# Kernel optimization log

Hardware: AMD Instinct MI355X
Metric: run time of the kernel (lower is better)

## Reference

```python
import jax, jax.numpy as jnp
import numpy as np

CL = 32
NUM_OBJ = 128
BATCH = 16
NUM_ROLLOUT = 8

def _linear(key, din, dout):
    k1, k2 = jax.random.split(key)
    s = 1.0 / np.sqrt(din)
    w = jax.random.uniform(k1, (din, dout), jnp.float32, -s, s)
    b = jax.random.uniform(k2, (dout,), jnp.float32, -s, s)
    return w, b

def setup_inputs() -> dict:
    key = jax.random.key(0)
    ks = jax.random.split(key, 16)
    cl = CL
    inp = {}
    inp['x'] = jax.random.normal(ks[0], (BATCH, 4, NUM_OBJ, 4), jnp.float32)
    inp['se_w'], inp['se_b'] = _linear(ks[1], 4, cl)
    inp['sc0_w'], inp['sc0_b'] = _linear(ks[2], cl, cl)
    inp['sc1_w'], inp['sc1_b'] = _linear(ks[3], cl, cl)
    inp['rc0_w'], inp['rc0_b'] = _linear(ks[4], 3 + 2 * cl, 2 * cl)
    inp['rc1_w'], inp['rc1_b'] = _linear(ks[5], 2 * cl, cl)
    inp['rc2_w'], inp['rc2_b'] = _linear(ks[6], cl, cl)
    inp['at0_w'], inp['at0_b'] = _linear(ks[7], 3 + 2 * cl, 2 * cl)
    inp['at1_w'], inp['at1_b'] = _linear(ks[8], 2 * cl, cl)
    inp['at2_w'], inp['at2_b'] = _linear(ks[9], cl, 1)
    inp['af0_w'], inp['af0_b'] = _linear(ks[10], cl, cl)
    inp['af1_w'], inp['af1_b'] = _linear(ks[11], cl, cl)
    inp['af2_w'], inp['af2_b'] = _linear(ks[12], cl, cl)
    inp['o0_w'], inp['o0_b'] = _linear(ks[13], 2 * cl, cl)
    inp['o1_w'], inp['o1_b'] = _linear(ks[14], cl, cl)
    inp['num_rollout'] = NUM_ROLLOUT
    return inp

def reference(x, se_w, se_b, sc0_w, sc0_b, sc1_w, sc1_b,
              rc0_w, rc0_b, rc1_w, rc1_b, rc2_w, rc2_b,
              at0_w, at0_b, at1_w, at1_b, at2_w, at2_b,
              af0_w, af0_b, af1_w, af1_b, af2_w, af2_b,
              o0_w, o0_b, o1_w, o1_b, num_rollout):
    n, _, o, _ = x.shape
    cl = sc0_w.shape[0]
    diag_mask = (1.0 - jnp.eye(o, dtype=x.dtype))[None, :, :, None]  # (1,o,o,1)

    def core(s):
        # s: (n, o, cl) -- interaction network core
        h1 = jax.nn.relu(s @ sc0_w + sc0_b)
        self_dyn = h1 @ sc1_w + sc1_b + h1
        a1 = jnp.broadcast_to(s[:, :, None, :], (n, o, o, cl))  # sender
        a2 = jnp.broadcast_to(s[:, None, :, :], (n, o, o, cl))  # receiver
        delta_xy = a1[..., :2] - a2[..., :2]
        dist = jnp.sqrt(jnp.sum(delta_xy ** 2, -1, keepdims=True) + 1e-10)
        comb = jnp.concatenate([a1, a2, dist, delta_xy], -1)  # (n,o,o,2cl+3)
        r1 = jax.nn.relu(comb @ rc0_w + rc0_b)
        r2 = jax.nn.relu(r1 @ rc1_w + rc1_b)
        rel = r2 @ rc2_w + rc2_b + r2
        att = jnp.tanh(comb @ at0_w + at0_b)
        att = jnp.tanh(att @ at1_w + at1_b)
        att = jnp.exp(att @ at2_w + at2_b)  # (n,o,o,1)
        rel = rel * (diag_mask * att)
        rel_dyn = jnp.sum(rel, axis=2)  # (n,o,cl)
        dyn = self_dyn + rel_dyn
        aff1 = jnp.tanh(dyn @ af0_w + af0_b)
        aff2 = jnp.tanh(aff1 @ af1_w + af1_b) + aff1
        aff3 = aff2 @ af2_w + af2_b
        aff_s = jnp.concatenate([aff3, s], -1)
        out1 = jnp.tanh(aff_s @ o0_w + o0_b)
        res = out1 @ o1_w + o1_b + out1
        res = res.at[..., :2].add(s[..., :2])
        return res

    # visual=False path: encode raw states
    latent = (x @ se_w + se_b)[..., 4:]            # (n,4,o,cl-4)
    state_codes = jnp.concatenate([x, latent], -1)  # (n,4,o,cl)
    present_states = state_codes[..., :4]
    cur = state_codes[:, -1]

    def step(s, _):
        s2 = core(s)
        return s2, s2

    _, rollouts = jax.lax.scan(step, cur, None, length=num_rollout)  # (R,n,o,cl)
    rollout_states = jnp.transpose(rollouts, (1, 0, 2, 3))[..., :4]
    return rollout_states, present_states
```

## Files before the change

kernel.cpp:

```cpp
#include <hip/hip_runtime.h>
#include <math.h>

#define NB 16
#define NOBJ 128
#define NROLL 8

typedef short bfrag __attribute__((ext_vector_type(8)));
typedef float f4t  __attribute__((ext_vector_type(4)));

struct W {
  const float *rc0w,*rc0b,*rc1w,*rc1b,*rc2w,*rc2b;
  const float *at0w,*at0b,*at1w,*at1b,*at2w,*at2b;
  const float *af0w,*af0b,*af1w,*af1b,*af2w,*af2b;
  const float *o0w,*o0b,*o1w,*o1b;
  const float *sc0w,*sc0b,*sc1w,*sc1b;
};

__device__ __forceinline__ float fast_tanh(float x){
  float e = __expf(2.f * x);
  return 1.f - __fdividef(2.f, e + 1.f);
}

__device__ __forceinline__ unsigned f2bf(float f){
  unsigned u = __float_as_uint(f);
  u = u + 0x7fffu + ((u >> 16) & 1u);
  return u >> 16;
}

__device__ __forceinline__ unsigned cvt_pk_bf16(float lo, float hi){
  unsigned r;
  asm("v_cvt_pk_bf16_f32 %0, %1, %2" : "=v"(r) : "v"(lo), "v"(hi));
  return r;
}

__global__ __launch_bounds__(512)
void pack_kernel(const float* __restrict__ at1w, const float* __restrict__ rc1w,
                 uint4* __restrict__ fragbuf)
{
  int t = threadIdx.x;
  int lane = t & 63, kt = (t>>6)&1, nt = (t>>7)&1, path = t>>8;
  const float* src = path ? rc1w : at1w;
  int c16 = lane & 15, qg = lane >> 4;
  unsigned r[4];
  #pragma unroll
  for (int e2 = 0; e2 < 4; e2++){
    int k0 = kt*32 + qg*8 + e2*2;
    unsigned lo = f2bf(src[k0*32     + nt*16 + c16]);
    unsigned hi = f2bf(src[(k0+1)*32 + nt*16 + c16]);
    r[e2] = lo | (hi << 16);
  }
  uint4 v; v.x=r[0]; v.y=r[1]; v.z=r[2]; v.w=r[3];
  fragbuf[((path*2+nt)*2+kt)*64 + lane] = v;
}

__global__ __launch_bounds__(128)
void encode_kernel(const float* __restrict__ x, const float* __restrict__ sew,
                   const float* __restrict__ seb, float* __restrict__ present,
                   float* __restrict__ S0)
{
  int bt = blockIdx.x;
  int o  = threadIdx.x;
  const float* xv = x + (size_t)(bt * NOBJ + o) * 4;
  float x0 = xv[0], x1 = xv[1], x2 = xv[2], x3 = xv[3];
  float* pr = present + (size_t)(bt * NOBJ + o) * 4;
  pr[0] = x0; pr[1] = x1; pr[2] = x2; pr[3] = x3;
  int t = bt & 3, b = bt >> 2;
  if (t == 3) {
    float* s = S0 + (size_t)(b * NOBJ + o) * 32;
    s[0] = x0; s[1] = x1; s[2] = x2; s[3] = x3;
    #pragma unroll
    for (int k = 4; k < 32; k++)
      s[k] = seb[k] + x0*sew[k] + x1*sew[32+k] + x2*sew[64+k] + x3*sew[96+k];
  }
}

__device__ void project_body(int tid, int bo, const float* __restrict__ s_sh,
                             float* __restrict__ h_sh, const W& w,
                             float* __restrict__ SD,
                             float* __restrict__ P1R, float* __restrict__ P1A,
                             float* __restrict__ P2AR,
                             float* __restrict__ PX, float* __restrict__ PY)
{
  int b = bo >> 7, o = bo & 127;
  if (tid < 64) {
    float a1r = w.rc0b[tid], a2r = 0.f, a1a = w.at0b[tid], a2a = 0.f;
    #pragma unroll
    for (int c = 0; c < 32; c++) {
      float sv = s_sh[c];
      a1r += sv * w.rc0w[c*64 + tid];
      a2r += sv * w.rc0w[(32+c)*64 + tid];
      a1a += sv * w.at0w[c*64 + tid];
      a2a += sv * w.at0w[(32+c)*64 + tid];
    }
    P1R[(size_t)bo*64 + tid] = a1r;
    P1A[(size_t)bo*64 + tid] = a1a;
    float2 p; p.x = a2a; p.y = a2r;
    ((float2*)P2AR)[(size_t)(b*64 + tid)*NOBJ + o] = p;
  }
  if (tid < 32) {
    float acc = w.sc0b[tid];
    #pragma unroll
    for (int c = 0; c < 32; c++) acc += s_sh[c] * w.sc0w[c*32 + tid];
    h_sh[tid] = fmaxf(acc, 0.f);
  }
  __syncthreads();
  if (tid < 32) {
    float acc = w.sc1b[tid] + h_sh[tid];
    #pragma unroll
    for (int c = 0; c < 32; c++) acc += h_sh[c] * w.sc1w[c*32 + tid];
    SD[(size_t)bo*32 + tid] = acc;
  }
  if (tid == 0) { PX[bo] = s_sh[0]; PY[bo] = s_sh[1]; }
}

__global__ __launch_bounds__(64)
void project_kernel(const float* __restrict__ S, W w,
                    float* SD, float* P1R, float* P1A,
                    float* P2AR, float* PX, float* PY)
{
  __shared__ float s_sh[32], h_sh[32];
  int bo = blockIdx.x, tid = threadIdx.x;
  if (tid < 32) s_sh[tid] = S[(size_t)bo*32 + tid];
  __syncthreads();
  project_body(tid, bo, s_sh, h_sh, w, SD, P1R, P1A, P2AR, PX, PY);
}

#define GEMM_PASS(BF, COUT) do {                                              \
  _Pragma("unroll")                                                           \
  for (int mt = 0; mt < 4; mt++){                                             \
    int jr = (wv<<6) + (mt<<4) + c16;                                         \
    bfrag a0 = *((const bfrag*)((const char*)smem + (jr<<7) + (((qg  ) ^ (jr&7))<<4))); \
    bfrag a1 = *((const bfrag*)((const char*)smem + (jr<<7) + (((4+qg) ^ (jr&7))<<4))); \
    _Pragma("unroll")                                                         \
    for (int nt = 0; nt < 2; nt++){                                           \
      COUT[mt][nt] = __builtin_amdgcn_mfma_f32_16x16x32_bf16(a0, BF[nt][0], COUT[mt][nt], 0,0,0); \
      COUT[mt][nt] = __builtin_amdgcn_mfma_f32_16x16x32_bf16(a1, BF[nt][1], COUT[mt][nt], 0,0,0); \
    }                                                                         \
  }                                                                           \
} while(0)

__global__ __launch_bounds__(128)
void step_kernel(const float* __restrict__ S_in,  const float* __restrict__ SD_in,
                 const float* __restrict__ P1R_in, const float* __restrict__ P1A_in,
                 const float* __restrict__ P2AR_in,
                 const float* __restrict__ PX_in,  const float* __restrict__ PY_in,
                 float* __restrict__ S_out, float* __restrict__ SD_out,
                 float* __restrict__ P1R_out, float* __restrict__ P1A_out,
                 float* __restrict__ P2AR_out,
                 float* __restrict__ PX_out, float* __restrict__ PY_out,
                 const uint4* __restrict__ fragbuf,
                 W w, float* __restrict__ out_roll, int tstep)
{
  __shared__ __align__(16) float smem[4352];
  float* qbuf    = smem + 4096;
  float* v0_sh   = smem + 4164;
  float* v1_sh   = smem + 4196;
  float* v2_sh   = smem + 4228;
  float* snew_sh = smem + 4260;
  float* h_sh    = smem + 4292;

  int bi = blockIdx.x;
  int b = bi >> 7, i = bi & 127;
  int tid = threadIdx.x;
  int j = tid;
  int wv = tid >> 6, l = tid & 63;
  int c16 = l & 15, qg = l >> 4;

  float px_i = S_in[(size_t)bi*32 + 0], py_i = S_in[(size_t)bi*32 + 1];
  float px_j = PX_in[b*NOBJ + j], py_j = PY_in[b*NOBJ + j];
  float dx = px_i - px_j, dy = py_i - py_j;
  float dist = sqrtf(dx*dx + dy*dy + 1e-10f);

  const float2* p2p = ((const float2*)P2AR_in) + (size_t)(b*64)*NOBJ + j;

  bfrag bfA[2][2];
  #pragma unroll
  for (int nt = 0; nt < 2; nt++)
    #pragma unroll
    for (int kt = 0; kt < 2; kt++)
      bfA[nt][kt] = *((const bfrag*)&fragbuf[(nt*2+kt)*64 + l]);

  unsigned relpk[32];
  {
    const float* p1a_ = P1A_in + (size_t)bi*64;
    const float* p1r_ = P1R_in + (size_t)bi*64;
    const float* gA = w.at0w + 64*64;
    const float* gR = w.rc0w + 64*64;
    #pragma unroll
    for (int s = 0; s < 8; s++){
      unsigned aw[4];
      #pragma unroll
      for (int e2 = 0; e2 < 4; e2++){
        int k0 = s*8 + e2*2, k1 = k0 + 1;
        float2 pa0 = p2p[(size_t)k0*NOBJ];
        float2 pa1 = p2p[(size_t)k1*NOBJ];
        float preA0 = p1a_[k0] + pa0.x + dist*gA[k0] + dx*gA[64+k0] + dy*gA[128+k0];
        float preA1 = p1a_[k1] + pa1.x + dist*gA[k1] + dx*gA[64+k1] + dy*gA[128+k1];
        float preR0 = p1r_[k0] + pa0.y + dist*gR[k0] + dx*gR[64+k0] + dy*gR[128+k0];
        float preR1 = p1r_[k1] + pa1.y + dist*gR[k1] + dx*gR[64+k1] + dy*gR[128+k1];
        float aA0 = fast_tanh(preA0), aA1 = fast_tanh(preA1);
        float aR0 = fmaxf(preR0, 0.f), aR1 = fmaxf(preR1, 0.f);
        aw[e2] = cvt_pk_bf16(aA0, aA1);
        relpk[s*4 + e2] = cvt_pk_bf16(aR0, aR1);
      }
      uint4 pk; pk.x=aw[0]; pk.y=aw[1]; pk.z=aw[2]; pk.w=aw[3];
      *((uint4*)((char*)smem + (j<<7) + ((s ^ (j&7))<<4))) = pk;
    }
  }
  __syncthreads();

  f4t cA[4][2];
  #pragma unroll
  for (int mt = 0; mt < 4; mt++)
    #pragma unroll
    for (int nt = 0; nt < 2; nt++) cA[mt][nt] = (f4t){0.f,0.f,0.f,0.f};
  GEMM_PASS(bfA, cA);
  __syncthreads();

  #pragma unroll
  for (int s = 0; s < 8; s++){
    uint4 pk; pk.x=relpk[s*4]; pk.y=relpk[s*4+1]; pk.z=relpk[s*4+2]; pk.w=relpk[s*4+3];
    *((uint4*)((char*)smem + (j<<7) + ((s ^ (j&7))<<4))) = pk;
  }

  float attv[16];
  {
    float bA0 = w.at1b[c16], bA1 = w.at1b[16 + c16];
    float w20 = w.at2w[c16], w21 = w.at2w[16 + c16];
    float a2b = w.at2b[0];
    #pragma unroll
    for (int mt = 0; mt < 4; mt++)
      #pragma unroll
      for (int reg = 0; reg < 4; reg++) {
        float s = fast_tanh(cA[mt][0][reg] + bA0) * w20
                + fast_tanh(cA[mt][1][reg] + bA1) * w21;
        s += __shfl_xor(s, 1); s += __shfl_xor(s, 2);
        s += __shfl_xor(s, 4); s += __shfl_xor(s, 8);
        int jj = wv*64 + mt*16 + qg*4 + reg;
        attv[mt*4 + reg] = (jj == i) ? 0.f : __expf(s + a2b);
      }
  }

  bfrag bfR[2][2];
  #pragma unroll
  for (int nt = 0; nt < 2; nt++)
    #pragma unroll
    for (int kt = 0; kt < 2; kt++)
      bfR[nt][kt] = *((const bfrag*)&fragbuf[(4 + nt*2+kt)*64 + l]);
  __syncthreads();

  f4t cR[4][2];
  #pragma unroll
  for (int mt = 0; mt < 4; mt++)
    #pragma unroll
    for (int nt = 0; nt < 2; nt++) cR[mt][nt] = (f4t){0.f,0.f,0.f,0.f};
  GEMM_PASS(bfR, cR);

  {
    float bR0 = w.rc1b[c16], bR1 = w.rc1b[16 + c16];
    float q0 = 0.f, q1 = 0.f, Ap = 0.f;
    #pragma unroll
    for (int mt = 0; mt < 4; mt++)
      #pragma unroll
      for (int reg = 0; reg < 4; reg++) {
        float av = attv[mt*4 + reg]; Ap += av;
        q0 += av * fmaxf(cR[mt][0][reg] + bR0, 0.f);
        q1 += av * fmaxf(cR[mt][1][reg] + bR1, 0.f);
      }
    q0 += __shfl_xor(q0, 16); q0 += __shfl_xor(q0, 32);
    q1 += __shfl_xor(q1, 16); q1 += __shfl_xor(q1, 32);
    Ap += __shfl_xor(Ap, 16); Ap += __shfl_xor(Ap, 32);
    if (l < 16) { qbuf[wv*33 + l] = q0; qbuf[wv*33 + 16 + l] = q1; }
    if (l == 0) qbuf[wv*33 + 32] = Ap;
  }
  __syncthreads();

  if (tid < 32) v2_sh[tid] = qbuf[tid] + qbuf[33 + tid];
  __syncthreads();
  if (tid < 32) {
    float A = qbuf[32] + qbuf[65];
    float acc = SD_in[(size_t)bi*32 + tid] + A * w.rc2b[tid] + v2_sh[tid];
    for (int k = 0; k < 32; k++) acc += v2_sh[k] * w.rc2w[k*32 + tid];
    v0_sh[tid] = acc;
  }
  __syncthreads();
  if (tid < 32) {
    float acc = w.af0b[tid];
    for (int k = 0; k < 32; k++) acc += v0_sh[k] * w.af0w[k*32 + tid];
    v1_sh[tid] = fast_tanh(acc);
  }
  __syncthreads();
  if (tid < 32) {
    float acc = w.af1b[tid];
    for (int k = 0; k < 32; k++) acc += v1_sh[k] * w.af1w[k*32 + tid];
    v2_sh[tid] = fast_tanh(acc) + v1_sh[tid];
  }
  __syncthreads();
  if (tid < 32) {
    float acc = w.af2b[tid];
    for (int k = 0; k < 32; k++) acc += v2_sh[k] * w.af2w[k*32 + tid];
    v0_sh[tid] = acc;
  }
  __syncthreads();
  if (tid < 32) {
    float acc = w.o0b[tid];
    for (int k = 0; k < 32; k++) acc += v0_sh[k] * w.o0w[k*32 + tid];
    for (int k = 0; k < 32; k++) acc += S_in[(size_t)bi*32 + k] * w.o0w[(32+k)*32 + tid];
    v1_sh[tid] = fast_tanh(acc);
  }
  __syncthreads();
  if (tid < 32) {
    float acc = w.o1b[tid] + v1_sh[tid];
    for (int k = 0; k < 32; k++) acc += v1_sh[k] * w.o1w[k*32 + tid];
    if (tid < 2) acc += S_in[(size_t)bi*32 + tid];
    snew_sh[tid] = acc;
    S_out[(size_t)bi*32 + tid] = acc;
    if (tid < 4)
      out_roll[(size_t)((b*NROLL + tstep)*NOBJ + i)*4 + tid] = acc;
  }
  __syncthreads();

  project_body(tid, bi, snew_sh, h_sh, w,
               SD_out, P1R_out, P1A_out, P2AR_out, PX_out, PY_out);
}

extern "C" void kernel_launch(void* const* d_in, const int* in_sizes, int n_in,
                              void* d_out, int out_size, void* d_ws, size_t ws_size,
                              hipStream_t stream)
{
  const float* x    = (const float*)d_in[0];
  const float* sew  = (const float*)d_in[1];
  const float* seb  = (const float*)d_in[2];
  W w;
  w.sc0w=(const float*)d_in[3];  w.sc0b=(const float*)d_in[4];
  w.sc1w=(const float*)d_in[5];  w.sc1b=(const float*)d_in[6];
  w.rc0w=(const float*)d_in[7];  w.rc0b=(const float*)d_in[8];
  w.rc1w=(const float*)d_in[9];  w.rc1b=(const float*)d_in[10];
  w.rc2w=(const float*)d_in[11]; w.rc2b=(const float*)d_in[12];
  w.at0w=(const float*)d_in[13]; w.at0b=(const float*)d_in[14];
  w.at1w=(const float*)d_in[15]; w.at1b=(const float*)d_in[16];
  w.at2w=(const float*)d_in[17]; w.at2b=(const float*)d_in[18];
  w.af0w=(const float*)d_in[19]; w.af0b=(const float*)d_in[20];
  w.af1w=(const float*)d_in[21]; w.af1b=(const float*)d_in[22];
  w.af2w=(const float*)d_in[23]; w.af2b=(const float*)d_in[24];
  w.o0w =(const float*)d_in[25]; w.o0b =(const float*)d_in[26];
  w.o1w =(const float*)d_in[27]; w.o1b =(const float*)d_in[28];

  float* out = (float*)d_out;
  float* out_roll    = out;
  float* out_present = out + NB*NROLL*NOBJ*4;

  float* ws = (float*)d_ws;
  size_t off = 0;
  auto alloc = [&](size_t n){ float* p = ws + off; off += n; return p; };
  float* S[2]    = { alloc(NB*NOBJ*32),   alloc(NB*NOBJ*32) };
  float* SD[2]   = { alloc(NB*NOBJ*32),   alloc(NB*NOBJ*32) };
  float* P1R[2]  = { alloc(NB*NOBJ*64),   alloc(NB*NOBJ*64) };
  float* P1A[2]  = { alloc(NB*NOBJ*64),   alloc(NB*NOBJ*64) };
  float* P2AR[2] = { alloc(NB*64*NOBJ*2), alloc(NB*64*NOBJ*2) };
  float* PX[2]   = { alloc(NB*NOBJ),      alloc(NB*NOBJ) };
  float* PY[2]   = { alloc(NB*NOBJ),      alloc(NB*NOBJ) };
  uint4* fragbuf = (uint4*)alloc(512 * 4);
  (void)ws_size; (void)in_sizes; (void)n_in; (void)out_size;

  hipLaunchKernelGGL(pack_kernel, dim3(1), dim3(512), 0, stream,
                     w.at1w, w.rc1w, fragbuf);
  hipLaunchKernelGGL(encode_kernel, dim3(NB*4), dim3(NOBJ), 0, stream,
                     x, sew, seb, out_present, S[0]);
  hipLaunchKernelGGL(project_kernel, dim3(NB*NOBJ), dim3(64), 0, stream,
                     S[0], w, SD[0], P1R[0], P1A[0], P2AR[0], PX[0], PY[0]);

  for (int t = 0; t < NROLL; t++) {
    int a = t & 1, oo = 1 - a;
    hipLaunchKernelGGL(step_kernel, dim3(NB*NOBJ), dim3(128), 0, stream,
                       S[a], SD[a], P1R[a], P1A[a], P2AR[a], PX[a], PY[a],
                       S[oo], SD[oo], P1R[oo], P1A[oo], P2AR[oo], PX[oo], PY[oo],
                       fragbuf, w, out_roll, t);
  }
}
```

Baseline: 405.6 us.

## Process two receiver objects per block to share sender-side loads

```diff
diff --git a/kernel.cpp b/kernel.cpp
--- a/kernel.cpp
+++ b/kernel.cpp
@@ -17,8 +17,8 @@
 };
 
 __device__ __forceinline__ float fast_tanh(float x){
-  float e = __expf(2.f * x);
-  return 1.f - __fdividef(2.f, e + 1.f);
+  float e = exp2f(x * 2.8853900817779268f);
+  return fmaf(__builtin_amdgcn_rcpf(e + 1.f), -2.f, 1.f);
 }
 
 __device__ __forceinline__ unsigned f2bf(float f){
@@ -74,7 +74,7 @@
   }
 }
 
-__device__ void project_body(int tid, int bo, const float* __restrict__ s_sh,
+__device__ void project_body(int pt, int bo, const float* __restrict__ s_sh,
                              float* __restrict__ h_sh, const W& w,
                              float* __restrict__ SD,
                              float* __restrict__ P1R, float* __restrict__ P1A,
@@ -82,35 +82,35 @@
                              float* __restrict__ PX, float* __restrict__ PY)
 {
   int b = bo >> 7, o = bo & 127;
-  if (tid < 64) {
-    float a1r = w.rc0b[tid], a2r = 0.f, a1a = w.at0b[tid], a2a = 0.f;
+  if (pt < 64) {
+    float a1r = w.rc0b[pt], a2r = 0.f, a1a = w.at0b[pt], a2a = 0.f;
     #pragma unroll
     for (int c = 0; c < 32; c++) {
       float sv = s_sh[c];
-      a1r += sv * w.rc0w[c*64 + tid];
-      a2r += sv * w.rc0w[(32+c)*64 + tid];
-      a1a += sv * w.at0w[c*64 + tid];
-      a2a += sv * w.at0w[(32+c)*64 + tid];
+      a1r += sv * w.rc0w[c*64 + pt];
+      a2r += sv * w.rc0w[(32+c)*64 + pt];
+      a1a += sv * w.at0w[c*64 + pt];
+      a2a += sv * w.at0w[(32+c)*64 + pt];
     }
-    P1R[(size_t)bo*64 + tid] = a1r;
-    P1A[(size_t)bo*64 + tid] = a1a;
-    float2 p; p.x = a2a; p.y = a2r;
-    ((float2*)P2AR)[(size_t)(b*64 + tid)*NOBJ + o] = p;
-  }
-  if (tid < 32) {
-    float acc = w.sc0b[tid];
-    #pragma unroll
-    for (int c = 0; c < 32; c++) acc += s_sh[c] * w.sc0w[c*32 + tid];
-    h_sh[tid] = fmaxf(acc, 0.f);
-  }
-  __syncthreads();
-  if (tid < 32) {
-    float acc = w.sc1b[tid] + h_sh[tid];
-    #pragma unroll
-    for (int c = 0; c < 32; c++) acc += h_sh[c] * w.sc1w[c*32 + tid];
-    SD[(size_t)bo*32 + tid] = acc;
-  }
-  if (tid == 0) { PX[bo] = s_sh[0]; PY[bo] = s_sh[1]; }
+    P1R[(size_t)bo*64 + pt] = a1r;
+    P1A[(size_t)bo*64 + pt] = a1a;
+    float2 pp; pp.x = a2a; pp.y = a2r;
+    ((float2*)P2AR)[(size_t)(b*64 + pt)*NOBJ + o] = pp;
+  }
+  if (pt < 32) {
+    float acc = w.sc0b[pt];
+    #pragma unroll
+    for (int c = 0; c < 32; c++) acc += s_sh[c] * w.sc0w[c*32 + pt];
+    h_sh[pt] = fmaxf(acc, 0.f);
+  }
+  __syncthreads();
+  if (pt < 32) {
+    float acc = w.sc1b[pt] + h_sh[pt];
+    #pragma unroll
+    for (int c = 0; c < 32; c++) acc += h_sh[c] * w.sc1w[c*32 + pt];
+    SD[(size_t)bo*32 + pt] = acc;
+  }
+  if (pt == 0) { PX[bo] = s_sh[0]; PY[bo] = s_sh[1]; }
 }
 
 __global__ __launch_bounds__(64)
@@ -125,12 +125,13 @@
   project_body(tid, bo, s_sh, h_sh, w, SD, P1R, P1A, P2AR, PX, PY);
 }
 
-#define GEMM_PASS(BF, COUT) do {                                              \
+#define GEMM_PASS(TBASE, BF, COUT) do {                                       \
   _Pragma("unroll")                                                           \
   for (int mt = 0; mt < 4; mt++){                                             \
-    int jr = (wv<<6) + (mt<<4) + c16;                                         \
-    bfrag a0 = *((const bfrag*)((const char*)smem + (jr<<7) + (((qg  ) ^ (jr&7))<<4))); \
-    bfrag a1 = *((const bfrag*)((const char*)smem + (jr<<7) + (((4+qg) ^ (jr&7))<<4))); \
+    int jr = (wv2<<6) + (mt<<4) + c16;                                        \
+    const char* rb = (const char*)(TBASE) + (jr<<7);                          \
+    bfrag a0 = *((const bfrag*)(rb + (((qg  ) ^ (jr&7))<<4)));                \
+    bfrag a1 = *((const bfrag*)(rb + (((4+qg) ^ (jr&7))<<4)));                \
     _Pragma("unroll")                                                         \
     for (int nt = 0; nt < 2; nt++){                                           \
       COUT[mt][nt] = __builtin_amdgcn_mfma_f32_16x16x32_bf16(a0, BF[nt][0], COUT[mt][nt], 0,0,0); \
@@ -139,7 +140,7 @@
   }                                                                           \
 } while(0)
 
-__global__ __launch_bounds__(128)
+__global__ __launch_bounds__(256)
 void step_kernel(const float* __restrict__ S_in,  const float* __restrict__ SD_in,
                  const float* __restrict__ P1R_in, const float* __restrict__ P1A_in,
                  const float* __restrict__ P2AR_in,
@@ -151,27 +152,24 @@
                  const uint4* __restrict__ fragbuf,
                  W w, float* __restrict__ out_roll, int tstep)
 {
-  __shared__ __align__(16) float smem[4352];
-  float* qbuf    = smem + 4096;
-  float* v0_sh   = smem + 4164;
-  float* v1_sh   = smem + 4196;
-  float* v2_sh   = smem + 4228;
-  float* snew_sh = smem + 4260;
-  float* h_sh    = smem + 4292;
-
-  int bi = blockIdx.x;
-  int b = bi >> 7, i = bi & 127;
+  __shared__ __align__(16) float smem[8644];
+  float* qb_base = smem + 8192;
+  float* vb_base = smem + 8324;
+
   int tid = threadIdx.x;
-  int j = tid;
-  int wv = tid >> 6, l = tid & 63;
-  int c16 = l & 15, qg = l >> 4;
-
-  float px_i = S_in[(size_t)bi*32 + 0], py_i = S_in[(size_t)bi*32 + 1];
-  float px_j = PX_in[b*NOBJ + j], py_j = PY_in[b*NOBJ + j];
-  float dx = px_i - px_j, dy = py_i - py_j;
-  float dist = sqrtf(dx*dx + dy*dy + 1e-10f);
-
-  const float2* p2p = ((const float2*)P2AR_in) + (size_t)(b*64)*NOBJ + j;
+  int g   = tid >> 7;
+  int lt  = tid & 127;
+  int w4  = tid >> 6;
+  int obj = w4 >> 1;
+  int wv2 = w4 & 1;
+  int l = tid & 63, c16 = l & 15, qg = l >> 4;
+
+  int p = blockIdx.x & 63, b = blockIdx.x >> 6;
+  int i0 = 2*p;
+  int bi0 = b*NOBJ + i0, bi1 = bi0 + 1;
+
+  char* t0 = (char*)smem;
+  char* t1 = (char*)smem + 16384;
 
   bfrag bfA[2][2];
   #pragma unroll
@@ -180,49 +178,79 @@
     for (int kt = 0; kt < 2; kt++)
       bfA[nt][kt] = *((const bfrag*)&fragbuf[(nt*2+kt)*64 + l]);
 
-  unsigned relpk[32];
-  {
-    const float* p1a_ = P1A_in + (size_t)bi*64;
-    const float* p1r_ = P1R_in + (size_t)bi*64;
-    const float* gA = w.at0w + 64*64;
-    const float* gR = w.rc0w + 64*64;
-    #pragma unroll
-    for (int s = 0; s < 8; s++){
-      unsigned aw[4];
-      #pragma unroll
-      for (int e2 = 0; e2 < 4; e2++){
-        int k0 = s*8 + e2*2, k1 = k0 + 1;
-        float2 pa0 = p2p[(size_t)k0*NOBJ];
-        float2 pa1 = p2p[(size_t)k1*NOBJ];
-        float preA0 = p1a_[k0] + pa0.x + dist*gA[k0] + dx*gA[64+k0] + dy*gA[128+k0];
-        float preA1 = p1a_[k1] + pa1.x + dist*gA[k1] + dx*gA[64+k1] + dy*gA[128+k1];
-        float preR0 = p1r_[k0] + pa0.y + dist*gR[k0] + dx*gR[64+k0] + dy*gR[128+k0];
-        float preR1 = p1r_[k1] + pa1.y + dist*gR[k1] + dx*gR[64+k1] + dy*gR[128+k1];
-        float aA0 = fast_tanh(preA0), aA1 = fast_tanh(preA1);
-        float aR0 = fmaxf(preR0, 0.f), aR1 = fmaxf(preR1, 0.f);
-        aw[e2] = cvt_pk_bf16(aA0, aA1);
-        relpk[s*4 + e2] = cvt_pk_bf16(aR0, aR1);
-      }
-      uint4 pk; pk.x=aw[0]; pk.y=aw[1]; pk.z=aw[2]; pk.w=aw[3];
-      *((uint4*)((char*)smem + (j<<7) + ((s ^ (j&7))<<4))) = pk;
+  float px0 = S_in[(size_t)bi0*32 + 0], py0 = S_in[(size_t)bi0*32 + 1];
+  float px1 = S_in[(size_t)bi1*32 + 0], py1 = S_in[(size_t)bi1*32 + 1];
+  float px_j = PX_in[b*NOBJ + lt], py_j = PY_in[b*NOBJ + lt];
+  float dx0 = px0 - px_j, dy0 = py0 - py_j;
+  float dx1 = px1 - px_j, dy1 = py1 - py_j;
+  float dist0 = sqrtf(dx0*dx0 + dy0*dy0 + 1e-10f);
+  float dist1 = sqrtf(dx1*dx1 + dy1*dy1 + 1e-10f);
+
+  const float2* p2p = ((const float2*)P2AR_in) + (size_t)(b*64)*NOBJ + lt;
+  const float* p1a0 = P1A_in + (size_t)bi0*64;
+  const float* p1r0 = P1R_in + (size_t)bi0*64;
+  const float* p1a1 = P1A_in + (size_t)bi1*64;
+  const float* p1r1 = P1R_in + (size_t)bi1*64;
+  const float* gA = w.at0w + 64*64;
+  const float* gR = w.rc0w + 64*64;
+
+  unsigned relpk[2][16];
+  #pragma unroll
+  for (int sl = 0; sl < 4; sl++){
+    unsigned aw0[4], aw1[4];
+    #pragma unroll
+    for (int e2 = 0; e2 < 4; e2++){
+      int k0 = g*32 + sl*8 + e2*2, k1 = k0 + 1;
+      float2 pa0 = p2p[(size_t)k0*NOBJ];
+      float2 pa1 = p2p[(size_t)k1*NOBJ];
+      float gA0=gA[k0], gA1=gA[64+k0], gA2=gA[128+k0];
+      float gB0=gA[k1], gB1=gA[64+k1], gB2=gA[128+k1];
+      float hA0=gR[k0], hA1=gR[64+k0], hA2=gR[128+k0];
+      float hB0=gR[k1], hB1=gR[64+k1], hB2=gR[128+k1];
+      float a00 = fast_tanh(p1a0[k0] + pa0.x + dist0*gA0 + dx0*gA1 + dy0*gA2);
+      float a01 = fast_tanh(p1a0[k1] + pa1.x + dist0*gB0 + dx0*gB1 + dy0*gB2);
+      float r00 = fmaxf(p1r0[k0] + pa0.y + dist0*hA0 + dx0*hA1 + dy0*hA2, 0.f);
+      float r01 = fmaxf(p1r0[k1] + pa1.y + dist0*hB0 + dx0*hB1 + dy0*hB2, 0.f);
+      aw0[e2] = cvt_pk_bf16(a00, a01);
+      relpk[0][sl*4 + e2] = cvt_pk_bf16(r00, r01);
+      float a10 = fast_tanh(p1a1[k0] + pa0.x + dist1*gA0 + dx1*gA1 + dy1*gA2);
+      float a11 = fast_tanh(p1a1[k1] + pa1.x + dist1*gB0 + dx1*gB1 + dy1*gB2);
+      float r10 = fmaxf(p1r1[k0] + pa0.y + dist1*hA0 + dx1*hA1 + dy1*hA2, 0.f);
+      float r11 = fmaxf(p1r1[k1] + pa1.y + dist1*hB0 + dx1*hB1 + dy1*hB2, 0.f);
+      aw1[e2] = cvt_pk_bf16(a10, a11);
+      relpk[1][sl*4 + e2] = cvt_pk_bf16(r10, r11);
     }
-  }
-  __syncthreads();
-
+    int s = g*4 + sl;
+    unsigned off = (lt<<7) + ((s ^ (lt&7))<<4);
+    uint4 pk0; pk0.x=aw0[0]; pk0.y=aw0[1]; pk0.z=aw0[2]; pk0.w=aw0[3];
+    uint4 pk1; pk1.x=aw1[0]; pk1.y=aw1[1]; pk1.z=aw1[2]; pk1.w=aw1[3];
+    *((uint4*)(t0 + off)) = pk0;
+    *((uint4*)(t1 + off)) = pk1;
+  }
+  __syncthreads();
+
+  const char* mytile = (const char*)smem + (obj<<14);
   f4t cA[4][2];
   #pragma unroll
   for (int mt = 0; mt < 4; mt++)
     #pragma unroll
     for (int nt = 0; nt < 2; nt++) cA[mt][nt] = (f4t){0.f,0.f,0.f,0.f};
-  GEMM_PASS(bfA, cA);
-  __syncthreads();
-
-  #pragma unroll
-  for (int s = 0; s < 8; s++){
-    uint4 pk; pk.x=relpk[s*4]; pk.y=relpk[s*4+1]; pk.z=relpk[s*4+2]; pk.w=relpk[s*4+3];
-    *((uint4*)((char*)smem + (j<<7) + ((s ^ (j&7))<<4))) = pk;
-  }
-
+  GEMM_PASS(mytile, bfA, cA);
+  __syncthreads();
+
+  #pragma unroll
+  for (int sl = 0; sl < 4; sl++){
+    int s = g*4 + sl;
+    unsigned off = (lt<<7) + ((s ^ (lt&7))<<4);
+    uint4 pk0; pk0.x=relpk[0][sl*4]; pk0.y=relpk[0][sl*4+1];
+               pk0.z=relpk[0][sl*4+2]; pk0.w=relpk[0][sl*4+3];
+    uint4 pk1; pk1.x=relpk[1][sl*4]; pk1.y=relpk[1][sl*4+1];
+               pk1.z=relpk[1][sl*4+2]; pk1.w=relpk[1][sl*4+3];
+    *((uint4*)(t0 + off)) = pk0;
+    *((uint4*)(t1 + off)) = pk1;
+  }
+
+  int i_self = i0 + obj;
   float attv[16];
   {
     float bA0 = w.at1b[c16], bA1 = w.at1b[16 + c16];
@@ -236,8 +264,8 @@
                 + fast_tanh(cA[mt][1][reg] + bA1) * w21;
         s += __shfl_xor(s, 1); s += __shfl_xor(s, 2);
         s += __shfl_xor(s, 4); s += __shfl_xor(s, 8);
-        int jj = wv*64 + mt*16 + qg*4 + reg;
-        attv[mt*4 + reg] = (jj == i) ? 0.f : __expf(s + a2b);
+        int jj = wv2*64 + mt*16 + qg*4 + reg;
+        attv[mt*4 + reg] = (jj == i_self) ? 0.f : __expf(s + a2b);
       }
   }
 
@@ -254,7 +282,7 @@
   for (int mt = 0; mt < 4; mt++)
     #pragma unroll
     for (int nt = 0; nt < 2; nt++) cR[mt][nt] = (f4t){0.f,0.f,0.f,0.f};
-  GEMM_PASS(bfR, cR);
+  GEMM_PASS(mytile, bfR, cR);
 
   {
     float bR0 = w.rc1b[c16], bR1 = w.rc1b[16 + c16];
@@ -270,57 +298,67 @@
     q0 += __shfl_xor(q0, 16); q0 += __shfl_xor(q0, 32);
     q1 += __shfl_xor(q1, 16); q1 += __shfl_xor(q1, 32);
     Ap += __shfl_xor(Ap, 16); Ap += __shfl_xor(Ap, 32);
-    if (l < 16) { qbuf[wv*33 + l] = q0; qbuf[wv*33 + 16 + l] = q1; }
-    if (l == 0) qbuf[wv*33 + 32] = Ap;
-  }
-  __syncthreads();
-
-  if (tid < 32) v2_sh[tid] = qbuf[tid] + qbuf[33 + tid];
-  __syncthreads();
-  if (tid < 32) {
-    float A = qbuf[32] + qbuf[65];
-    float acc = SD_in[(size_t)bi*32 + tid] + A * w.rc2b[tid] + v2_sh[tid];
-    for (int k = 0; k < 32; k++) acc += v2_sh[k] * w.rc2w[k*32 + tid];
-    v0_sh[tid] = acc;
-  }
-  __syncthreads();
-  if (tid < 32) {
-    float acc = w.af0b[tid];
-    for (int k = 0; k < 32; k++) acc += v0_sh[k] * w.af0w[k*32 + tid];
-    v1_sh[tid] = fast_tanh(acc);
-  }
-  __syncthreads();
-  if (tid < 32) {
-    float acc = w.af1b[tid];
-    for (int k = 0; k < 32; k++) acc += v1_sh[k] * w.af1w[k*32 + tid];
-    v2_sh[tid] = fast_tanh(acc) + v1_sh[tid];
-  }
-  __syncthreads();
-  if (tid < 32) {
-    float acc = w.af2b[tid];
-    for (int k = 0; k < 32; k++) acc += v2_sh[k] * w.af2w[k*32 + tid];
-    v0_sh[tid] = acc;
-  }
-  __syncthreads();
-  if (tid < 32) {
-    float acc = w.o0b[tid];
-    for (int k = 0; k < 32; k++) acc += v0_sh[k] * w.o0w[k*32 + tid];
-    for (int k = 0; k < 32; k++) acc += S_in[(size_t)bi*32 + k] * w.o0w[(32+k)*32 + tid];
-    v1_sh[tid] = fast_tanh(acc);
-  }
-  __syncthreads();
-  if (tid < 32) {
-    float acc = w.o1b[tid] + v1_sh[tid];
-    for (int k = 0; k < 32; k++) acc += v1_sh[k] * w.o1w[k*32 + tid];
-    if (tid < 2) acc += S_in[(size_t)bi*32 + tid];
-    snew_sh[tid] = acc;
-    S_out[(size_t)bi*32 + tid] = acc;
-    if (tid < 4)
-      out_roll[(size_t)((b*NROLL + tstep)*NOBJ + i)*4 + tid] = acc;
-  }
-  __syncthreads();
-
-  project_body(tid, bi, snew_sh, h_sh, w,
+    float* qb = qb_base + obj*66;
+    if (l < 16) { qb[wv2*33 + l] = q0; qb[wv2*33 + 16 + l] = q1; }
+    if (l == 0) qb[wv2*33 + 32] = Ap;
+  }
+  __syncthreads();
+
+  int og = tid >> 7, pt = tid & 127;
+  int bio = bi0 + og;
+  float* qbo  = qb_base + og*66;
+  float* v0_sh = vb_base + og*160;
+  float* v1_sh = v0_sh + 32;
+  float* v2_sh = v0_sh + 64;
+  float* snew_sh = v0_sh + 96;
+  float* h_sh = v0_sh + 128;
+
+  if (pt < 32) v2_sh[pt] = qbo[pt] + qbo[33 + pt];
+  __syncthreads();
+  if (pt < 32) {
+    float A = qbo[32] + qbo[65];
+    float acc = SD_in[(size_t)bio*32 + pt] + A * w.rc2b[pt] + v2_sh[pt];
+    for (int k = 0; k < 32; k++) acc += v2_sh[k] * w.rc2w[k*32 + pt];
+    v0_sh[pt] = acc;
+  }
+  __syncthreads();
+  if (pt < 32) {
+    float acc = w.af0b[pt];
+    for (int k = 0; k < 32; k++) acc += v0_sh[k] * w.af0w[k*32 + pt];
+    v1_sh[pt] = fast_tanh(acc);
+  }
+  __syncthreads();
+  if (pt < 32) {
+    float acc = w.af1b[pt];
+    for (int k = 0; k < 32; k++) acc += v1_sh[k] * w.af1w[k*32 + pt];
+    v2_sh[pt] = fast_tanh(acc) + v1_sh[pt];
+  }
+  __syncthreads();
+  if (pt < 32) {
+    float acc = w.af2b[pt];
+    for (int k = 0; k < 32; k++) acc += v2_sh[k] * w.af2w[k*32 + pt];
+    v0_sh[pt] = acc;
+  }
+  __syncthreads();
+  if (pt < 32) {
+    float acc = w.o0b[pt];
+    for (int k = 0; k < 32; k++) acc += v0_sh[k] * w.o0w[k*32 + pt];
+    for (int k = 0; k < 32; k++) acc += S_in[(size_t)bio*32 + k] * w.o0w[(32+k)*32 + pt];
+    v1_sh[pt] = fast_tanh(acc);
+  }
+  __syncthreads();
+  if (pt < 32) {
+    float acc = w.o1b[pt] + v1_sh[pt];
+    for (int k = 0; k < 32; k++) acc += v1_sh[k] * w.o1w[k*32 + pt];
+    if (pt < 2) acc += S_in[(size_t)bio*32 + pt];
+    snew_sh[pt] = acc;
+    S_out[(size_t)bio*32 + pt] = acc;
+    if (pt < 4)
+      out_roll[(size_t)((b*NROLL + tstep)*NOBJ + (i_self - obj + og))*4 + pt] = acc;
+  }
+  __syncthreads();
+
+  project_body(pt, bio, snew_sh, h_sh, w,
                SD_out, P1R_out, P1A_out, P2AR_out, PX_out, PY_out);
 }
 
@@ -372,7 +410,7 @@
 
   for (int t = 0; t < NROLL; t++) {
     int a = t & 1, oo = 1 - a;
-    hipLaunchKernelGGL(step_kernel, dim3(NB*NOBJ), dim3(128), 0, stream,
+    hipLaunchKernelGGL(step_kernel, dim3(NB*NOBJ/2), dim3(256), 0, stream,
                        S[a], SD[a], P1R[a], P1A[a], P2AR[a], PX[a], PY[a],
                        S[oo], SD[oo], P1R[oo], P1A[oo], P2AR[oo], PX[oo], PY[oo],
                        fragbuf, w, out_roll, t);
```

After: 405.5 us. No clear change (-0.0%).
